# Kernel tuning notes

Hardware: AMD Instinct MI355X
Metric: run time of the kernel (lower is better)

## Reference

```python
import jax, jax.numpy as jnp
import numpy as np

D = 128
H = 256


def setup_inputs() -> dict:
    key = jax.random.key(0)
    ks = jax.random.split(key, 16)
    B, T = 512, 128
    C = D + H + D  # combined = [x, h, mask]
    stdv_c = 1.0 / np.sqrt(C)
    stdv_d = 1.0 / np.sqrt(D)
    stdv_h = 1.0 / np.sqrt(H)
    u = lambda k, shape, s: jax.random.uniform(k, shape, jnp.float32, -s, s)
    return {
        "input": jax.random.normal(ks[0], (B, 4, T, D), jnp.float32),
        "X_mean": jax.random.normal(ks[1], (1, T, D), jnp.float32),
        "zl_w": u(ks[2], (H, C), stdv_c), "zl_b": u(ks[3], (H,), stdv_c),
        "rl_w": u(ks[4], (H, C), stdv_c), "rl_b": u(ks[5], (H,), stdv_c),
        "hl_w": u(ks[6], (H, C), stdv_c), "hl_b": u(ks[7], (H,), stdv_c),
        "gx_w": u(ks[8], (D, D), stdv_d), "gx_b": u(ks[9], (D,), stdv_d),
        "gh_w": u(ks[10], (H, D), stdv_d), "gh_b": u(ks[11], (H,), stdv_d),
        "fc_w": u(ks[12], (1, H), stdv_h), "fc_b": u(ks[13], (1,), stdv_h),
    }


def reference(input, X_mean, zl_w, zl_b, rl_w, rl_b, hl_w, hl_b,
              gx_w, gx_b, gh_w, gh_b, fc_w, fc_b):
    B = input.shape[0]
    # FilterLinear with identity filter: weight is masked to its diagonal
    gx_w_masked = gx_w * jnp.eye(D, dtype=gx_w.dtype)
    gx_diag = jnp.diagonal(gx_w_masked)  # elementwise equivalent

    # split channels and move time to leading axis for scan: [T, B, D]
    X = jnp.moveaxis(input[:, 0], 1, 0)
    X_last = jnp.moveaxis(input[:, 1], 1, 0)
    Mask = jnp.moveaxis(input[:, 2], 1, 0)
    Delta = jnp.moveaxis(input[:, 3], 1, 0)
    Xm = jnp.moveaxis(X_mean, 1, 0)  # [T, 1, D], broadcasts over batch

    h0 = jnp.zeros((B, H), jnp.float32)

    def step(h, inp):
        x, x_last, x_mean, m, d = inp
        delta_x = jnp.exp(-jax.nn.relu(d * gx_diag + gx_b))          # [B, D]
        delta_h = jnp.exp(-jax.nn.relu(d @ gh_w.T + gh_b))           # [B, H]
        x = m * x + (1 - m) * (delta_x * x_last + (1 - delta_x) * x_mean)
        h = delta_h * h
        combined = jnp.concatenate([x, h, m], axis=1)                # [B, D+H+D]
        z = jax.nn.sigmoid(combined @ zl_w.T + zl_b)
        r = jax.nn.sigmoid(combined @ rl_w.T + rl_b)
        combined_r = jnp.concatenate([x, r * h, m], axis=1)
        h_tilde = jnp.tanh(combined_r @ hl_w.T + hl_b)
        h = (1 - z) * h + z * h_tilde
        return h, h

    _, hs = jax.lax.scan(step, h0, (X, X_last, Xm, Mask, Delta))     # [T, B, H]
    outputs = jnp.moveaxis(hs, 0, 1)                                 # [B, T, H]
    # num_class == 2, output_last == False: binary head on all steps
    out = jax.nn.sigmoid(outputs @ fc_w.T + fc_b)                    # [B, T, 1]
    return out.astype(jnp.float32)
```

## Files before the change

### kernel.cpp

```cpp
#include <hip/hip_runtime.h>
#include <hip/hip_bf16.h>
#include <cstdint>

typedef unsigned int u32;
typedef unsigned short u16;
typedef __attribute__((ext_vector_type(8))) short bf16x8;
typedef __attribute__((ext_vector_type(4))) float f32x4;

#define TT 128
#define BB 512
#define DD 128
#define HH 256
#define CC 512

#define HDA_OFF 32768
#define PA_OFF  34816

#define BAR() do { asm volatile("s_waitcnt lgkmcnt(0)" ::: "memory"); \
                   __builtin_amdgcn_s_barrier(); \
                   asm volatile("" ::: "memory"); } while(0)

__device__ __forceinline__ u16 f2bf(float f){
  u32 u = __builtin_bit_cast(u32, f);
  u += 0x7FFFu + ((u >> 16) & 1u);
  return (u16)(u >> 16);
}
__device__ __forceinline__ float bf1(u16 w){ return __builtin_bit_cast(float, ((u32)w) << 16); }
__device__ __forceinline__ float sigm(float x){ return 1.f / (1.f + __expf(-x)); }
__device__ __forceinline__ float tanh_fast(float x){
  float t = __expf(-2.f * fabsf(x));
  float r = (1.f - t) / (1.f + t);
  return copysignf(r, x);
}

__global__ __launch_bounds__(256) void prep_weights(
    const float* __restrict__ zl_w, const float* __restrict__ rl_w,
    const float* __restrict__ hl_w, const float* __restrict__ gh_w,
    const float* __restrict__ gx_w,
    u32* __restrict__ zlB, u32* __restrict__ rlB, u32* __restrict__ hlF,
    u32* __restrict__ Bpre, u32* __restrict__ ghF, float* __restrict__ gxd){
  int gid = blockIdx.x * 256 + threadIdx.x;
  if (gid < 32768){
    int d   = gid & 3;
    int l   = (gid >> 2) & 63;
    int kt  = (gid >> 8) & 7;
    int ntg = (gid >> 11) & 15;
    int nn  = 16*ntg + (l & 15);
    int kk  = 32*kt + 8*(l >> 4) + 2*d;
    int c0 = 128 + kk;
    zlB[gid] = (u32)f2bf(zl_w[nn*CC + c0]) | ((u32)f2bf(zl_w[nn*CC + c0 + 1]) << 16);
    rlB[gid] = (u32)f2bf(rl_w[nn*CC + c0]) | ((u32)f2bf(rl_w[nn*CC + c0 + 1]) << 16);
    hlF[gid] = (u32)f2bf(hl_w[nn*CC + c0]) | ((u32)f2bf(hl_w[nn*CC + c0 + 1]) << 16);
  }
  #pragma unroll
  for (int q = 0; q < 2; ++q){
    int id = q*65536 + gid;
    if (id < 98304){
      int d2 = id & 3;
      int l  = (id >> 2) & 63;
      int kt = (id >> 8) & 7;
      int nt = id >> 11;
      int g  = nt >> 4;
      int nc = (nt & 15)*16 + (l & 15);
      int k  = 32*kt + 8*(l >> 4) + 2*d2;
      int sc = (k < 128) ? k : k + 256;
      const float* W = (g == 0) ? zl_w : ((g == 1) ? rl_w : hl_w);
      Bpre[id] = (u32)f2bf(W[nc*CC + sc]) | ((u32)f2bf(W[nc*CC + sc + 1]) << 16);
    }
  }
  if (gid < 16384){
    int d2 = gid & 3;
    int l  = (gid >> 2) & 63;
    int kt = (gid >> 8) & 3;
    int nt = gid >> 10;
    int nc = nt*16 + (l & 15);
    int k  = 32*kt + 8*(l >> 4) + 2*d2;
    ghF[gid] = (u32)f2bf(gh_w[nc*DD + k]) | ((u32)f2bf(gh_w[nc*DD + k + 1]) << 16);
  }
  if (gid < 128) gxd[gid] = gx_w[gid*DD + gid];
}

__global__ __launch_bounds__(512, 2) void precompute_mfma(
    const float* __restrict__ input, const float* __restrict__ xmean,
    const float* __restrict__ gxd, const float* __restrict__ gx_b,
    const float* __restrict__ zl_b, const float* __restrict__ rl_b,
    const float* __restrict__ hl_b, const float* __restrict__ gh_b,
    const u32* __restrict__ Bpre, const u32* __restrict__ ghF,
    float* __restrict__ zpre, float* __restrict__ rpre, float* __restrict__ hpre,
    float* __restrict__ dh){
  __shared__ __align__(16) u16 A1[4][8][64][8];
  __shared__ __align__(16) u16 A2[4][4][64][8];
  const int tid = threadIdx.x;
  const int r0 = blockIdx.x * 64;
  const int t  = r0 >> 9;
  const int b0 = r0 & 511;
  {
    int row = tid >> 3, dsg = tid & 7, d0 = dsg * 16;
    int b = b0 + row;
    const size_t ib = ((size_t)b * 4 * TT + t) * DD;
    int mt = row >> 4;
    #pragma unroll
    for (int gg = 0; gg < 2; ++gg){
      int db = d0 + 8*gg;
      float xv[8], lv[8], mv[8], dv[8], xm[8], gd[8], gb[8];
      #pragma unroll
      for (int q = 0; q < 2; ++q){
        *(float4*)&xv[q*4] = *(const float4*)&input[ib + 0*TT*DD + db + q*4];
        *(float4*)&lv[q*4] = *(const float4*)&input[ib + 1*TT*DD + db + q*4];
        *(float4*)&mv[q*4] = *(const float4*)&input[ib + 2*TT*DD + db + q*4];
        *(float4*)&dv[q*4] = *(const float4*)&input[ib + 3*TT*DD + db + q*4];
        *(float4*)&xm[q*4] = *(const float4*)&xmean[t*DD + db + q*4];
        *(float4*)&gd[q*4] = *(const float4*)&gxd[db + q*4];
        *(float4*)&gb[q*4] = *(const float4*)&gx_b[db + q*4];
      }
      union { u16 s[8]; bf16x8 v; } pe, pm, pd;
      #pragma unroll
      for (int j = 0; j < 8; ++j){
        float dxv = __expf(-fmaxf(dv[j]*gd[j] + gb[j], 0.f));
        float xe  = mv[j]*xv[j] + (1.f - mv[j])*(dxv*lv[j] + (1.f - dxv)*xm[j]);
        pe.s[j] = f2bf(xe);
        pm.s[j] = f2bf(mv[j]);
        pd.s[j] = f2bf(dv[j]);
      }
      int kt1 = db >> 5;
      int l1  = (row & 15) + 16*((db >> 3) & 3);
      *(bf16x8*)&A1[mt][kt1][l1][0]     = pe.v;
      *(bf16x8*)&A1[mt][4 + kt1][l1][0] = pm.v;
      *(bf16x8*)&A2[mt][kt1][l1][0]     = pd.v;
    }
  }
  __syncthreads();
  const int l = tid & 63, w = tid >> 6;
  const int wm = w >> 2, wn = w & 3;
  const int rowl = 4 * (l >> 4), coll = l & 15;
  f32x4 acc[2][12];
  #pragma unroll
  for (int m = 0; m < 2; ++m)
    #pragma unroll
    for (int i = 0; i < 12; ++i) acc[m][i] = (f32x4){0.f,0.f,0.f,0.f};
  #pragma unroll
  for (int kt = 0; kt < 8; ++kt){
    bf16x8 a0 = *(const bf16x8*)&A1[wm*2 + 0][kt][l][0];
    bf16x8 a1 = *(const bf16x8*)&A1[wm*2 + 1][kt][l][0];
    #pragma unroll
    for (int i = 0; i < 12; ++i){
      int nt = wn*12 + i;
      bf16x8 bf = *(const bf16x8*)(Bpre + ((nt*8 + kt)*64 + l)*4);
      acc[0][i] = __builtin_amdgcn_mfma_f32_16x16x32_bf16(a0, bf, acc[0][i], 0, 0, 0);
      acc[1][i] = __builtin_amdgcn_mfma_f32_16x16x32_bf16(a1, bf, acc[1][i], 0, 0, 0);
    }
  }
  #pragma unroll
  for (int m = 0; m < 2; ++m){
    int grow = r0 + wm*32 + m*16 + rowl;
    #pragma unroll
    for (int i = 0; i < 12; ++i){
      int nt = wn*12 + i;
      int g = nt >> 4;
      int lc = (nt & 15)*16 + coll;
      float bias; float* dst;
      if (g == 0){ dst = zpre; bias = zl_b[lc]; }
      else if (g == 1){ dst = rpre; bias = rl_b[lc]; }
      else { dst = hpre; bias = hl_b[lc]; }
      #pragma unroll
      for (int rg = 0; rg < 4; ++rg)
        dst[(size_t)(grow + rg)*HH + lc] = acc[m][i][rg] + bias;
    }
  }
  f32x4 ac2[2][4];
  #pragma unroll
  for (int m = 0; m < 2; ++m)
    #pragma unroll
    for (int i = 0; i < 4; ++i) ac2[m][i] = (f32x4){0.f,0.f,0.f,0.f};
  #pragma unroll
  for (int kt = 0; kt < 4; ++kt){
    bf16x8 a0 = *(const bf16x8*)&A2[wm*2 + 0][kt][l][0];
    bf16x8 a1 = *(const bf16x8*)&A2[wm*2 + 1][kt][l][0];
    #pragma unroll
    for (int i = 0; i < 4; ++i){
      int nt = wn*4 + i;
      bf16x8 bf = *(const bf16x8*)(ghF + ((nt*4 + kt)*64 + l)*4);
      ac2[0][i] = __builtin_amdgcn_mfma_f32_16x16x32_bf16(a0, bf, ac2[0][i], 0, 0, 0);
      ac2[1][i] = __builtin_amdgcn_mfma_f32_16x16x32_bf16(a1, bf, ac2[1][i], 0, 0, 0);
    }
  }
  #pragma unroll
  for (int m = 0; m < 2; ++m){
    int grow = r0 + wm*32 + m*16 + rowl;
    #pragma unroll
    for (int i = 0; i < 4; ++i){
      int lc = (wn*4 + i)*16 + coll;
      float bias = gh_b[lc];
      #pragma unroll
      for (int rg = 0; rg < 4; ++rg)
        dh[(size_t)(grow + rg)*HH + lc] = __expf(-fmaxf(ac2[m][i][rg] + bias, 0.f));
    }
  }
}

__global__ __launch_bounds__(512, 2) void recurrent_mfma(
    const float* __restrict__ zpre, const float* __restrict__ rpre,
    const float* __restrict__ hpre, const float* __restrict__ dh,
    const u32* __restrict__ zlB, const u32* __restrict__ rlB,
    const u32* __restrict__ hlF, u16* __restrict__ hout){
  __shared__ u32 smem[36864];
  const int tid = threadIdx.x;
  const int l = tid & 63, w = tid >> 6;
  const int b0 = blockIdx.x * 16;
  const int rowb = 4 * (l >> 4);
  const int col0 = 32*w + (l & 15);

  #pragma unroll
  for (int i = 0; i < 64; ++i) smem[i*512 + tid] = hlF[i*512 + tid];
  #pragma unroll
  for (int i = 0; i < 4; ++i) smem[HDA_OFF + i*512 + tid] = 0;

  bf16x8 zb[2][8], rb[2][8];
  #pragma unroll
  for (int nt = 0; nt < 2; ++nt){
    #pragma unroll
    for (int kt = 0; kt < 8; ++kt){
      int off = (((w*2 + nt)*8 + kt)*64 + l)*4;
      zb[nt][kt] = *(const bf16x8*)(zlB + off);
      rb[nt][kt] = *(const bf16x8*)(rlB + off);
    }
  }
  __syncthreads();

  int scb[2];
  #pragma unroll
  for (int nt = 0; nt < 2; ++nt)
    scb[nt] = w*512 + (2*nt + ((l >> 3) & 1))*128 + rowb*8 + (l & 7);

  float hdreg[2][4] = {{0.f,0.f,0.f,0.f},{0.f,0.f,0.f,0.f}};
  float zreg[2][4];

  u16* pa16 = (u16*)(smem + PA_OFF);
  u16* hd16 = (u16*)(smem + HDA_OFF);

  for (int t = 0; t < TT; ++t){
    float pz[2][4], pr[2][4], ph[2][4], pdh[2][4];
    int tn = (t < TT-1) ? t+1 : TT-1;
    #pragma unroll
    for (int nt = 0; nt < 2; ++nt){
      #pragma unroll
      for (int jr = 0; jr < 4; ++jr){
        size_t o  = ((size_t)t *BB + b0 + rowb + jr)*HH + col0 + 16*nt;
        size_t o2 = ((size_t)tn*BB + b0 + rowb + jr)*HH + col0 + 16*nt;
        pz[nt][jr]  = zpre[o];
        pr[nt][jr]  = rpre[o];
        ph[nt][jr]  = hpre[o];
        pdh[nt][jr] = dh[o2];
      }
    }
    f32x4 cz[2] = {{0.f,0.f,0.f,0.f},{0.f,0.f,0.f,0.f}};
    f32x4 cr[2] = {{0.f,0.f,0.f,0.f},{0.f,0.f,0.f,0.f}};
    #pragma unroll
    for (int kt = 0; kt < 8; ++kt){
      bf16x8 a = *(const bf16x8*)(smem + HDA_OFF + kt*256 + l*4);
      cz[0] = __builtin_amdgcn_mfma_f32_16x16x32_bf16(a, zb[0][kt], cz[0], 0, 0, 0);
      cz[1] = __builtin_amdgcn_mfma_f32_16x16x32_bf16(a, zb[1][kt], cz[1], 0, 0, 0);
      cr[0] = __builtin_amdgcn_mfma_f32_16x16x32_bf16(a, rb[0][kt], cr[0], 0, 0, 0);
      cr[1] = __builtin_amdgcn_mfma_f32_16x16x32_bf16(a, rb[1][kt], cr[1], 0, 0, 0);
    }
    #pragma unroll
    for (int nt = 0; nt < 2; ++nt){
      #pragma unroll
      for (int jr = 0; jr < 4; ++jr){
        float zv = sigm(pz[nt][jr] + cz[nt][jr]);
        float rv = sigm(pr[nt][jr] + cr[nt][jr]);
        zreg[nt][jr] = zv;
        pa16[scb[nt] + jr*8] = f2bf(rv * hdreg[nt][jr]);
      }
    }
    BAR();
    f32x4 ch[2] = {{0.f,0.f,0.f,0.f},{0.f,0.f,0.f,0.f}};
    #pragma unroll
    for (int kt = 0; kt < 8; ++kt){
      bf16x8 a  = *(const bf16x8*)(smem + PA_OFF + kt*256 + l*4);
      bf16x8 bh0 = *(const bf16x8*)(smem + ((2*w+0)*8 + kt)*256 + l*4);
      bf16x8 bh1 = *(const bf16x8*)(smem + ((2*w+1)*8 + kt)*256 + l*4);
      ch[0] = __builtin_amdgcn_mfma_f32_16x16x32_bf16(a, bh0, ch[0], 0, 0, 0);
      ch[1] = __builtin_amdgcn_mfma_f32_16x16x32_bf16(a, bh1, ch[1], 0, 0, 0);
    }
    #pragma unroll
    for (int nt = 0; nt < 2; ++nt){
      #pragma unroll
      for (int jr = 0; jr < 4; ++jr){
        float ht = tanh_fast(ph[nt][jr] + ch[nt][jr]);
        float hd = hdreg[nt][jr];
        float zv = zreg[nt][jr];
        float hn = (1.f - zv)*hd + zv*ht;
        size_t o = ((size_t)t*BB + b0 + rowb + jr)*HH + col0 + 16*nt;
        hout[o] = f2bf(hn);
        float hdn = pdh[nt][jr] * hn;
        hdreg[nt][jr] = hdn;
        hd16[scb[nt] + jr*8] = f2bf(hdn);
      }
    }
    BAR();
  }
}

__global__ __launch_bounds__(256) void head(const u16* __restrict__ hout,
    const float* __restrict__ fc_w, const float* __restrict__ fc_b,
    float* __restrict__ out){
  int w = threadIdx.x >> 6, lane = threadIdx.x & 63;
  int rr = blockIdx.x * 4 + w;
  const ushort4 hv = *(const ushort4*)&hout[(size_t)rr*HH + lane*4];
  const float4 fw = *(const float4*)&fc_w[lane*4];
  float s = bf1(hv.x)*fw.x + bf1(hv.y)*fw.y + bf1(hv.z)*fw.z + bf1(hv.w)*fw.w;
  #pragma unroll
  for (int o = 32; o >= 1; o >>= 1) s += __shfl_xor(s, o, 64);
  if (lane == 0){
    int t = rr >> 9, b = rr & 511;
    out[b*TT + t] = sigm(s + fc_b[0]);
  }
}

extern "C" void kernel_launch(void* const* d_in, const int* in_sizes, int n_in,
                              void* d_out, int out_size, void* d_ws, size_t ws_size,
                              hipStream_t stream) {
  const float* input = (const float*)d_in[0];
  const float* xmean = (const float*)d_in[1];
  const float* zl_w  = (const float*)d_in[2];
  const float* zl_b  = (const float*)d_in[3];
  const float* rl_w  = (const float*)d_in[4];
  const float* rl_b  = (const float*)d_in[5];
  const float* hl_w  = (const float*)d_in[6];
  const float* hl_b  = (const float*)d_in[7];
  const float* gx_w  = (const float*)d_in[8];
  const float* gx_b  = (const float*)d_in[9];
  const float* gh_w  = (const float*)d_in[10];
  const float* gh_b  = (const float*)d_in[11];
  const float* fc_w  = (const float*)d_in[12];
  const float* fc_b  = (const float*)d_in[13];
  float* out = (float*)d_out;

  const size_t S = (size_t)TT * BB * HH;
  float* zpre = (float*)d_ws;
  float* rpre = zpre + S;
  float* hpre = rpre + S;
  float* dhp  = hpre + S;
  u16*   hout = (u16*)(dhp + S);
  u32*   zlB  = (u32*)(hout + S);
  u32*   rlB  = zlB + 32768;
  u32*   hlF  = rlB + 32768;
  u32*   Bpre = hlF + 32768;
  u32*   ghF  = Bpre + 98304;
  float* gxd  = (float*)(ghF + 16384);

  prep_weights<<<256, 256, 0, stream>>>(zl_w, rl_w, hl_w, gh_w, gx_w,
                                        zlB, rlB, hlF, Bpre, ghF, gxd);
  precompute_mfma<<<1024, 512, 0, stream>>>(input, xmean, gxd, gx_b,
                                            zl_b, rl_b, hl_b, gh_b,
                                            Bpre, ghF,
                                            zpre, rpre, hpre, dhp);
  recurrent_mfma<<<32, 512, 0, stream>>>(zpre, rpre, hpre, dhp, zlB, rlB, hlF, hout);
  head<<<16384, 256, 0, stream>>>(hout, fc_w, fc_b, out);
}
```

Baseline: 887.7 us.

## Pack z/r preactivations as bf16 pairs and prefetch next step's inputs

The precompute kernel now stores z and r preactivations as one packed u32 of two bf16 values instead of two fp32 arrays, reordering MFMA tile assignment so each wave holds matching z and r columns. The recurrent kernel software-prefetches the next timestep's zr, hpre and delta_h values into registers before the current step's compute, hiding global load latency on the serial critical path. This lowers intermediate memory traffic and load count, at the cost of bf16 rounding of the z/r preactivations and more live registers.

```diff
diff --git a/kernel.cpp b/kernel.cpp
--- a/kernel.cpp
+++ b/kernel.cpp
@@ -25,6 +25,8 @@
   u += 0x7FFFu + ((u >> 16) & 1u);
   return (u16)(u >> 16);
 }
+__device__ __forceinline__ float bflo(u32 w){ return __builtin_bit_cast(float, w << 16); }
+__device__ __forceinline__ float bfhi(u32 w){ return __builtin_bit_cast(float, w & 0xFFFF0000u); }
 __device__ __forceinline__ float bf1(u16 w){ return __builtin_bit_cast(float, ((u32)w) << 16); }
 __device__ __forceinline__ float sigm(float x){ return 1.f / (1.f + __expf(-x)); }
 __device__ __forceinline__ float tanh_fast(float x){
@@ -86,8 +88,7 @@
     const float* __restrict__ zl_b, const float* __restrict__ rl_b,
     const float* __restrict__ hl_b, const float* __restrict__ gh_b,
     const u32* __restrict__ Bpre, const u32* __restrict__ ghF,
-    float* __restrict__ zpre, float* __restrict__ rpre, float* __restrict__ hpre,
-    float* __restrict__ dh){
+    u32* __restrict__ zrp, float* __restrict__ hpre, float* __restrict__ dh){
   __shared__ __align__(16) u16 A1[4][8][64][8];
   __shared__ __align__(16) u16 A2[4][4][64][8];
   const int tid = threadIdx.x;
@@ -144,7 +145,7 @@
     bf16x8 a1 = *(const bf16x8*)&A1[wm*2 + 1][kt][l][0];
     #pragma unroll
     for (int i = 0; i < 12; ++i){
-      int nt = wn*12 + i;
+      int nt = 4*i + wn;
       bf16x8 bf = *(const bf16x8*)(Bpre + ((nt*8 + kt)*64 + l)*4);
       acc[0][i] = __builtin_amdgcn_mfma_f32_16x16x32_bf16(a0, bf, acc[0][i], 0, 0, 0);
       acc[1][i] = __builtin_amdgcn_mfma_f32_16x16x32_bf16(a1, bf, acc[1][i], 0, 0, 0);
@@ -154,17 +155,22 @@
   for (int m = 0; m < 2; ++m){
     int grow = r0 + wm*32 + m*16 + rowl;
     #pragma unroll
-    for (int i = 0; i < 12; ++i){
-      int nt = wn*12 + i;
-      int g = nt >> 4;
-      int lc = (nt & 15)*16 + coll;
-      float bias; float* dst;
-      if (g == 0){ dst = zpre; bias = zl_b[lc]; }
-      else if (g == 1){ dst = rpre; bias = rl_b[lc]; }
-      else { dst = hpre; bias = hl_b[lc]; }
+    for (int i = 0; i < 4; ++i){
+      int lc = (4*i + wn)*16 + coll;
+      float bz = zl_b[lc], br = rl_b[lc];
+      #pragma unroll
+      for (int rg = 0; rg < 4; ++rg){
+        u32 pk = (u32)f2bf(acc[m][i][rg] + bz) | ((u32)f2bf(acc[m][i+4][rg] + br) << 16);
+        zrp[(size_t)(grow + rg)*HH + lc] = pk;
+      }
+    }
+    #pragma unroll
+    for (int i = 8; i < 12; ++i){
+      int lc = (4*(i-8) + wn)*16 + coll;
+      float bh = hl_b[lc];
       #pragma unroll
       for (int rg = 0; rg < 4; ++rg)
-        dst[(size_t)(grow + rg)*HH + lc] = acc[m][i][rg] + bias;
+        hpre[(size_t)(grow + rg)*HH + lc] = acc[m][i][rg] + bh;
     }
   }
   f32x4 ac2[2][4];
@@ -199,8 +205,8 @@
 }
 
 __global__ __launch_bounds__(512, 2) void recurrent_mfma(
-    const float* __restrict__ zpre, const float* __restrict__ rpre,
-    const float* __restrict__ hpre, const float* __restrict__ dh,
+    const u32* __restrict__ zrp, const float* __restrict__ hpre,
+    const float* __restrict__ dh,
     const u32* __restrict__ zlB, const u32* __restrict__ rlB,
     const u32* __restrict__ hlF, u16* __restrict__ hout){
   __shared__ u32 smem[36864];
@@ -238,19 +244,34 @@
   u16* pa16 = (u16*)(smem + PA_OFF);
   u16* hd16 = (u16*)(smem + HDA_OFF);
 
+  u32 zrC[2][4]; float phC[2][4], pdC[2][4];
+  #pragma unroll
+  for (int nt = 0; nt < 2; ++nt){
+    #pragma unroll
+    for (int jr = 0; jr < 4; ++jr){
+      size_t o  = ((size_t)b0 + rowb + jr)*HH + col0 + 16*nt;
+      size_t o2 = ((size_t)BB + b0 + rowb + jr)*HH + col0 + 16*nt;
+      zrC[nt][jr] = zrp[o];
+      phC[nt][jr] = hpre[o];
+      pdC[nt][jr] = dh[o2];
+    }
+  }
+
   for (int t = 0; t < TT; ++t){
-    float pz[2][4], pr[2][4], ph[2][4], pdh[2][4];
-    int tn = (t < TT-1) ? t+1 : TT-1;
-    #pragma unroll
-    for (int nt = 0; nt < 2; ++nt){
-      #pragma unroll
-      for (int jr = 0; jr < 4; ++jr){
-        size_t o  = ((size_t)t *BB + b0 + rowb + jr)*HH + col0 + 16*nt;
-        size_t o2 = ((size_t)tn*BB + b0 + rowb + jr)*HH + col0 + 16*nt;
-        pz[nt][jr]  = zpre[o];
-        pr[nt][jr]  = rpre[o];
-        ph[nt][jr]  = hpre[o];
-        pdh[nt][jr] = dh[o2];
+    u32 zrN[2][4]; float phN[2][4], pdN[2][4];
+    {
+      int tn  = (t < TT-1) ? t+1 : TT-1;
+      int tn2 = (t < TT-2) ? t+2 : TT-1;
+      #pragma unroll
+      for (int nt = 0; nt < 2; ++nt){
+        #pragma unroll
+        for (int jr = 0; jr < 4; ++jr){
+          size_t o  = ((size_t)tn *BB + b0 + rowb + jr)*HH + col0 + 16*nt;
+          size_t o2 = ((size_t)tn2*BB + b0 + rowb + jr)*HH + col0 + 16*nt;
+          zrN[nt][jr] = zrp[o];
+          phN[nt][jr] = hpre[o];
+          pdN[nt][jr] = dh[o2];
+        }
       }
     }
     f32x4 cz[2] = {{0.f,0.f,0.f,0.f},{0.f,0.f,0.f,0.f}};
@@ -267,8 +288,8 @@
     for (int nt = 0; nt < 2; ++nt){
       #pragma unroll
       for (int jr = 0; jr < 4; ++jr){
-        float zv = sigm(pz[nt][jr] + cz[nt][jr]);
-        float rv = sigm(pr[nt][jr] + cr[nt][jr]);
+        float zv = sigm(bflo(zrC[nt][jr]) + cz[nt][jr]);
+        float rv = sigm(bfhi(zrC[nt][jr]) + cr[nt][jr]);
         zreg[nt][jr] = zv;
         pa16[scb[nt] + jr*8] = f2bf(rv * hdreg[nt][jr]);
       }
@@ -287,18 +308,27 @@
     for (int nt = 0; nt < 2; ++nt){
       #pragma unroll
       for (int jr = 0; jr < 4; ++jr){
-        float ht = tanh_fast(ph[nt][jr] + ch[nt][jr]);
+        float ht = tanh_fast(phC[nt][jr] + ch[nt][jr]);
         float hd = hdreg[nt][jr];
         float zv = zreg[nt][jr];
         float hn = (1.f - zv)*hd + zv*ht;
         size_t o = ((size_t)t*BB + b0 + rowb + jr)*HH + col0 + 16*nt;
         hout[o] = f2bf(hn);
-        float hdn = pdh[nt][jr] * hn;
+        float hdn = pdC[nt][jr] * hn;
         hdreg[nt][jr] = hdn;
         hd16[scb[nt] + jr*8] = f2bf(hdn);
       }
     }
     BAR();
+    #pragma unroll
+    for (int nt = 0; nt < 2; ++nt){
+      #pragma unroll
+      for (int jr = 0; jr < 4; ++jr){
+        zrC[nt][jr] = zrN[nt][jr];
+        phC[nt][jr] = phN[nt][jr];
+        pdC[nt][jr] = pdN[nt][jr];
+      }
+    }
   }
 }
 
@@ -338,9 +368,8 @@
   float* out = (float*)d_out;
 
   const size_t S = (size_t)TT * BB * HH;
-  float* zpre = (float*)d_ws;
-  float* rpre = zpre + S;
-  float* hpre = rpre + S;
+  u32*   zrp  = (u32*)d_ws;
+  float* hpre = (float*)(zrp + S);
   float* dhp  = hpre + S;
   u16*   hout = (u16*)(dhp + S);
   u32*   zlB  = (u32*)(hout + S);
@@ -355,7 +384,7 @@
   precompute_mfma<<<1024, 512, 0, stream>>>(input, xmean, gxd, gx_b,
                                             zl_b, rl_b, hl_b, gh_b,
                                             Bpre, ghF,
-                                            zpre, rpre, hpre, dhp);
-  recurrent_mfma<<<32, 512, 0, stream>>>(zpre, rpre, hpre, dhp, zlB, rlB, hlF, hout);
+                                            zrp, hpre, dhp);
+  recurrent_mfma<<<32, 512, 0, stream>>>(zrp, hpre, dhp, zlB, rlB, hlF, hout);
   head<<<16384, 256, 0, stream>>>(hout, fc_w, fc_b, out);
 }
```

After: 753.8 us. -15.1%, faster.
